# Optimization experiments

Measured on AMD Instinct MI355X. Metric: run time of the kernel, lower is better.

## Reference

```python
import jax, jax.numpy as jnp
import numpy as np

TQ, TK, B, QD, KD, VD = 1024, 1024, 16, 1024, 1024, 1024

def setup_inputs() -> dict:
    key = jax.random.key(0)
    k1, k2, k3, k4, k5 = jax.random.split(key, 5)
    queries = jax.random.normal(k1, (TQ, B, QD), dtype=jnp.float32)
    keys = jax.random.normal(k2, (TK, B, KD), dtype=jnp.float32)
    values = jax.random.normal(k3, (TK, B, VD), dtype=jnp.float32)
    # torch Linear weight [out=key_dim, in=query_dim], uniform(-0.1, 0.1)
    W = jax.random.uniform(k4, (KD, QD), dtype=jnp.float32, minval=-0.1, maxval=0.1)
    # mask: True means position is masked out (filled with -inf)
    mask = jax.random.bernoulli(k5, 0.5, (TK, B))
    return {"queries": queries, "keys": keys, "values": values, "W": W, "mask": mask}

def reference(queries, keys, values, W, mask):
    # project queries: [Tq,B,QD] @ W.T -> [Tq,B,KD]
    q = jnp.einsum('tbq,kq->tbk', queries, W)
    # scores: [B,Tq,Tk]
    scores = jnp.einsum('tbk,sbk->bts', q, keys)
    # mask [Tk,B] -> [B,1,Tk]; True positions get -inf
    scores = jnp.where(mask.T[:, None, :], -jnp.inf, scores)
    attn = jax.nn.softmax(scores, axis=-1)  # [B,Tq,Tk]
    # output: [B,Tq,Vd] -> [Tq,B,Vd]
    x = jnp.einsum('bts,sbv->tbv', attn, values)
    # attn returned as [Tq,B,Tk] (matches torch .transpose(0,1))
    return x, jnp.transpose(attn, (1, 0, 2))
```

## Files before the change

kernel.cpp:

```cpp
#include <hip/hip_runtime.h>
#include <stdint.h>

#define TQd 1024
#define TKd 1024
#define Bd  16
#define QDd 1024
#define KDd 1024
#define VDd 1024
#define MROWS (TQd * Bd)

#define S_W   326390.0f
#define S_QIN 5021.4f
#define S_KIN 5021.4f
#define S_QP  2719.9f

typedef float f32x4 __attribute__((ext_vector_type(4)));
typedef short short8 __attribute__((ext_vector_type(8)));
typedef unsigned short u16x4 __attribute__((ext_vector_type(4)));
typedef int i32x4 __attribute__((ext_vector_type(4)));
typedef signed char i8x4 __attribute__((ext_vector_type(4)));

__device__ __forceinline__ unsigned short f2bf(float x) {
  unsigned u = __float_as_uint(x);
  u += 0x7FFFu + ((u >> 16) & 1u);
  return (unsigned short)(u >> 16);
}
__device__ __forceinline__ float bf2f(unsigned short h) {
  return __uint_as_float(((unsigned)h) << 16);
}

__device__ __forceinline__ char* lds_ptr(unsigned short* base, int r, int kcol) {
  int byte = (r << 7) + (kcol << 1);
  byte ^= (r & 7) << 4;
  return (char*)base + byte;
}
__device__ __forceinline__ i32x4 lds_fragi(const char* plane, int row, int chunk) {
  return *(const i32x4*)(plane + row * 128 + (((chunk) ^ (row & 7)) << 4));
}
__device__ __forceinline__ short8 lds_fragh(const char* plane, int row, int chunk) {
  return *(const short8*)(plane + row * 128 + (((chunk) ^ (row & 7)) << 4));
}

__device__ __forceinline__ void gload16(const void* g, void* l) {
  __builtin_amdgcn_global_load_lds(
      (const __attribute__((address_space(1))) void*)(uintptr_t)g,
      (__attribute__((address_space(3))) void*)(uintptr_t)l,
      16, 0, 0);
}

#define MFMA_BF16 __builtin_amdgcn_mfma_f32_16x16x32_bf16
#define MFMA_I8   __builtin_amdgcn_mfma_i32_16x16x64_i8
#define SBAR() __builtin_amdgcn_s_barrier()

__device__ __forceinline__ void q16split(float x, float scale, int& hi, int& lo) {
  float r = rintf(x * scale);
  r = fminf(fmaxf(r, -32639.f), 32639.f);
  int ri = (int)r;
  lo = (int)(signed char)(ri & 255);
  hi = (ri - lo) >> 8;
}

__global__ __launch_bounds__(256) void k_quant8(const float* __restrict__ src,
                                                signed char* __restrict__ hi,
                                                signed char* __restrict__ lo,
                                                int n4, float scale) {
  int i = blockIdx.x * 256 + threadIdx.x;
  int stride = gridDim.x * 256;
  for (; i < n4; i += stride) {
    f32x4 v = ((const f32x4*)src)[i];
    i8x4 h, l;
#pragma unroll
    for (int j = 0; j < 4; ++j) {
      int hj, lj;
      q16split(v[j], scale, hj, lj);
      h[j] = (signed char)hj;
      l[j] = (signed char)lj;
    }
    ((i8x4*)hi)[i] = h;
    ((i8x4*)lo)[i] = l;
  }
}

__global__ __launch_bounds__(256) void k_vt(const float* __restrict__ values,
                                            unsigned short* __restrict__ vt) {
  __shared__ unsigned short T[64 * 64];
  const int tid = threadIdx.x;
  const int b = blockIdx.z;
  const int s0 = blockIdx.y * 64, v0 = blockIdx.x * 64;
  const int sIdx = tid >> 4, vIdx = tid & 15;
  f32x4 rv[4];
#pragma unroll
  for (int j = 0; j < 4; ++j)
    rv[j] = *(const f32x4*)(values + (size_t)(s0 + sIdx * 4 + j) * (Bd * VDd) +
                            (size_t)b * VDd + v0 + vIdx * 4);
#pragma unroll
  for (int j2 = 0; j2 < 4; ++j2) {
    u16x4 w;
    w[0] = f2bf(rv[0][j2]); w[1] = f2bf(rv[1][j2]);
    w[2] = f2bf(rv[2][j2]); w[3] = f2bf(rv[3][j2]);
    int v = vIdx * 4 + j2;
    int byte = (v << 7) + (sIdx << 3);
    byte ^= (v & 7) << 4;
    *(u16x4*)((char*)T + byte) = w;
  }
  __syncthreads();
  const int l15 = tid & 15, lk = (tid >> 4) & 3, wv = tid >> 6;
  int row = wv * 16 + l15;
#pragma unroll
  for (int c = 0; c < 2; ++c) {
    int lc = lk + c * 4;
    int byte = (row << 7) + (((lc) ^ (row & 7)) << 4);
    short8 d = *(const short8*)((char*)T + byte);
    *(short8*)(vt + ((size_t)(b * 1024 + v0 + row)) * 1024 + s0 + lc * 8) = d;
  }
}

__device__ __forceinline__ void stage2_i8c(char* p, int kt,
    const signed char* ah, const signed char* al,
    const signed char* bh, const signed char* bl,
    int m0, int n0, int wv, int lane) {
  int rsub = lane >> 3;
  int lc = (lane & 7) ^ rsub;
  const signed char* A = (lc < 4) ? ah : al;
  const signed char* B = (lc < 4) ? bh : bl;
  int ke = kt + (lc & 3) * 16;
#pragma unroll
  for (int i = 0; i < 4; ++i) {
    int issue = wv * 4 + i;
    int row = issue * 8 + rsub;
    gload16(A + (size_t)(m0 + row) * 1024 + ke, p + issue * 1024);
    gload16(B + (size_t)(n0 + row) * 1024 + ke, p + 16384 + issue * 1024);
  }
}

__device__ __forceinline__ void stage2_i8s(char* p, int kt,
    const signed char* ah, const signed char* al,
    const signed char* bh, const signed char* bl,
    int t0, int s0, int b, int wv, int lane) {
  int rsub = lane >> 3;
  int lc = (lane & 7) ^ rsub;
  const signed char* A = (lc < 4) ? ah : al;
  const signed char* B = (lc < 4) ? bh : bl;
  int ke = kt + (lc & 3) * 16;
#pragma unroll
  for (int i = 0; i < 4; ++i) {
    int issue = wv * 4 + i;
    int row = issue * 8 + rsub;
    gload16(A + ((size_t)(t0 + row) * Bd + b) * 1024 + ke, p + issue * 1024);
    gload16(B + ((size_t)(s0 + row) * Bd + b) * 1024 + ke, p + 16384 + issue * 1024);
  }
}

#define GEMMI8_LOOP2(STAGEM)                                                  \
  const int tid = threadIdx.x;                                                \
  const int lane = tid & 63, wv = tid >> 6;                                   \
  const int wm = wv >> 1, wn = wv & 1;                                        \
  const int l15 = lane & 15, lk = lane >> 4;                                  \
  const i32x4 izero = {0, 0, 0, 0};                                           \
  i32x4 acc1[4][4], acc2[4][4];                                               \
  _Pragma("unroll") for (int m = 0; m < 4; ++m)                               \
  _Pragma("unroll") for (int n = 0; n < 4; ++n) {                             \
    acc1[m][n] = izero; acc2[m][n] = izero;                                   \
  }                                                                           \
  char* p0 = ldsbuf;                                                          \
  char* p1 = ldsbuf + 32768;                                                  \
  STAGEM(p0, 0);                                                              \
  asm volatile("s_waitcnt vmcnt(0)" ::: "memory");                            \
  SBAR();                                                                     \
  _Pragma("unroll 1") for (int h = 0; h < 16; ++h) {                          \
    if (h < 15) STAGEM(p1, (h + 1) * 64);                                     \
    i32x4 bh_[4], bl_[4], ah_[4], al_[4];                                     \
    _Pragma("unroll") for (int n = 0; n < 4; ++n) {                           \
      bh_[n] = lds_fragi(p0 + 16384, wn * 64 + n * 16 + l15, lk);             \
      bl_[n] = lds_fragi(p0 + 16384, wn * 64 + n * 16 + l15, 4 + lk);         \
    }                                                                         \
    _Pragma("unroll") for (int m = 0; m < 4; ++m) {                           \
      ah_[m] = lds_fragi(p0, wm * 64 + m * 16 + l15, lk);                     \
      al_[m] = lds_fragi(p0, wm * 64 + m * 16 + l15, 4 + lk);                 \
    }                                                                         \
    __builtin_amdgcn_s_setprio(1);                                            \
    _Pragma("unroll") for (int m = 0; m < 4; ++m)                             \
    _Pragma("unroll") for (int n = 0; n < 4; ++n) {                           \
      acc1[m][n] = MFMA_I8(ah_[m], bh_[n], acc1[m][n], 0, 0, 0);              \
      acc2[m][n] = MFMA_I8(ah_[m], bl_[n], acc2[m][n], 0, 0, 0);              \
      acc2[m][n] = MFMA_I8(al_[m], bh_[n], acc2[m][n], 0, 0, 0);              \
    }                                                                         \
    __builtin_amdgcn_s_setprio(0);                                            \
    if (h < 15) {                                                             \
      asm volatile("s_waitcnt vmcnt(0)" ::: "memory");                        \
      SBAR();                                                                 \
      char* pt = p0; p0 = p1; p1 = pt;                                        \
    }                                                                         \
  }

__global__ __launch_bounds__(256, 2) void k_qproj_i8(
    const signed char* __restrict__ Qh, const signed char* __restrict__ Ql,
    const signed char* __restrict__ Wh, const signed char* __restrict__ Wl,
    signed char* __restrict__ qh, signed char* __restrict__ ql) {
  __shared__ char ldsbuf[2 * 32768];
  int lin = blockIdx.x;
  int x = lin & 7, c = lin >> 3;
  const int m0 = (x * 16 + (c >> 3)) * 128, n0 = (c & 7) * 128;
#define STG_Q(P, KT) stage2_i8c(P, KT, Qh, Ql, Wh, Wl, m0, n0, wv, lane)
  GEMMI8_LOOP2(STG_Q)
#undef STG_Q
  const float inv = 1.0f / (S_QIN * S_W);
#pragma unroll
  for (int m = 0; m < 4; ++m)
#pragma unroll
    for (int n = 0; n < 4; ++n)
#pragma unroll
      for (int r = 0; r < 4; ++r) {
        int row = m0 + wm * 64 + m * 16 + lk * 4 + r;
        int col = n0 + wn * 64 + n * 16 + l15;
        float q = ((float)acc1[m][n][r] * 65536.f + (float)acc2[m][n][r] * 256.f) * inv;
        int hj, lj;
        q16split(q, S_QP, hj, lj);
        qh[(size_t)row * KDd + col] = (signed char)hj;
        ql[(size_t)row * KDd + col] = (signed char)lj;
      }
}

__global__ __launch_bounds__(256, 2) void k_scores_i8(
    const signed char* __restrict__ qh, const signed char* __restrict__ ql,
    const signed char* __restrict__ kh, const signed char* __restrict__ kl,
    float* __restrict__ sc) {
  __shared__ char ldsbuf[2 * 32768];
  int lin = blockIdx.x;
  int x = lin & 7, c = lin >> 3;
  const int b = x * 2 + (c >> 6);
  const int t0 = ((c >> 3) & 7) * 128, s0 = (c & 7) * 128;
#define STG_S(P, KT) stage2_i8s(P, KT, qh, ql, kh, kl, t0, s0, b, wv, lane)
  GEMMI8_LOOP2(STG_S)
#undef STG_S
  const float inv = 1.0f / (S_QP * S_KIN);
#pragma unroll
  for (int m = 0; m < 4; ++m)
#pragma unroll
    for (int n = 0; n < 4; ++n)
#pragma unroll
      for (int r = 0; r < 4; ++r) {
        int t = t0 + wm * 64 + m * 16 + lk * 4 + r;
        int s = s0 + wn * 64 + n * 16 + l15;
        float v = ((float)acc1[m][n][r] * 65536.f + (float)acc2[m][n][r] * 256.f) * inv;
        sc[((size_t)t * Bd + b) * TKd + s] = v;
      }
}

__global__ __launch_bounds__(256) void k_softmax2(float* __restrict__ attn,
                                                  const int* __restrict__ mask,
                                                  unsigned short* __restrict__ pb) {
  const int wv = threadIdx.x >> 6, lane = threadIdx.x & 63;
  const size_t r = (size_t)blockIdx.x * 4 + wv;
  const int b = (int)(r & 15);
  float* row = attn + r * TKd;
  unsigned short* prow = pb + r * TKd;

  f32x4 v[4];
  float m = -INFINITY;
#pragma unroll
  for (int c = 0; c < 4; ++c) {
    int s0 = (c * 64 + lane) * 4;
    v[c] = *(const f32x4*)(row + s0);
#pragma unroll
    for (int j = 0; j < 4; ++j) {
      if (mask[(size_t)(s0 + j) * Bd + b] != 0) v[c][j] = -INFINITY;
      m = fmaxf(m, v[c][j]);
    }
  }
#pragma unroll
  for (int off = 32; off > 0; off >>= 1) m = fmaxf(m, __shfl_xor(m, off));
  float sum = 0.f;
#pragma unroll
  for (int c = 0; c < 4; ++c)
#pragma unroll
    for (int j = 0; j < 4; ++j) {
      float e = expf(v[c][j] - m);
      v[c][j] = e;
      sum += e;
    }
#pragma unroll
  for (int off = 32; off > 0; off >>= 1) sum += __shfl_xor(sum, off);
  float inv = 1.f / sum;
#pragma unroll
  for (int c = 0; c < 4; ++c) {
    int s0 = (c * 64 + lane) * 4;
    u16x4 hb;
#pragma unroll
    for (int j = 0; j < 4; ++j) {
      v[c][j] *= inv;
      hb[j] = f2bf(v[c][j]);
    }
    *(f32x4*)(row + s0) = v[c];
    *(u16x4*)(prow + s0) = hb;
  }
}

__device__ __forceinline__ void stage2_pv(char* p, int st,
    const unsigned short* pb, const unsigned short* vtb,
    int t0, int v0, int b, int wv, int lane) {
  int rsub = lane >> 3;
  int lc = (lane & 7) ^ rsub;
  int ke = st + lc * 8;
#pragma unroll
  for (int i = 0; i < 4; ++i) {
    int issue = wv * 4 + i;
    int row = issue * 8 + rsub;
    gload16(pb + ((size_t)(t0 + row) * Bd + b) * 1024 + ke, p + issue * 1024);
    gload16(vtb + (size_t)(v0 + row) * 1024 + ke, p + 16384 + issue * 1024);
  }
}

__global__ __launch_bounds__(256, 2) void k_out3(const unsigned short* __restrict__ pb,
                                                 const unsigned short* __restrict__ vt,
                                                 float* __restrict__ xo) {
  __shared__ char ldsbuf[2 * 32768];
  int lin = blockIdx.x;
  int x = lin & 7, c = lin >> 3;
  const int b = x * 2 + (c >> 6);
  const int t0 = ((c >> 3) & 7) * 128, v0 = (c & 7) * 128;
  const unsigned short* vtb = vt + (size_t)b * VDd * TKd;

  const int tid = threadIdx.x;
  const int lane = tid & 63, wv = tid >> 6;
  const int wm = wv >> 1, wn = wv & 1;
  const int l15 = lane & 15, lk = lane >> 4;
  const f32x4 vzero = {0.f, 0.f, 0.f, 0.f};
  f32x4 acc[4][4];
#pragma unroll
  for (int m = 0; m < 4; ++m)
#pragma unroll
    for (int n = 0; n < 4; ++n) acc[m][n] = vzero;

  char* p0 = ldsbuf;
  char* p1 = ldsbuf + 32768;
#define STG_PV(P, ST) stage2_pv(P, ST, pb, vtb, t0, v0, b, wv, lane)
  STG_PV(p0, 0);
  asm volatile("s_waitcnt vmcnt(0)" ::: "memory");
  SBAR();
#pragma unroll 1
  for (int h = 0; h < 16; ++h) {
    if (h < 15) STG_PV(p1, (h + 1) * 64);
    short8 bf[4][2], af[4][2];
#pragma unroll
    for (int n = 0; n < 4; ++n)
#pragma unroll
      for (int kk = 0; kk < 2; ++kk)
        bf[n][kk] = lds_fragh(p0 + 16384, wn * 64 + n * 16 + l15, kk * 4 + lk);
#pragma unroll
    for (int m = 0; m < 4; ++m)
#pragma unroll
      for (int kk = 0; kk < 2; ++kk)
        af[m][kk] = lds_fragh(p0, wm * 64 + m * 16 + l15, kk * 4 + lk);
    __builtin_amdgcn_s_setprio(1);
#pragma unroll
    for (int m = 0; m < 4; ++m)
#pragma unroll
      for (int n = 0; n < 4; ++n)
#pragma unroll
        for (int kk = 0; kk < 2; ++kk)
          acc[m][n] = MFMA_BF16(af[m][kk], bf[n][kk], acc[m][n], 0, 0, 0);
    __builtin_amdgcn_s_setprio(0);
    if (h < 15) {
      asm volatile("s_waitcnt vmcnt(0)" ::: "memory");
      SBAR();
      char* pt = p0; p0 = p1; p1 = pt;
    }
  }
#undef STG_PV
#pragma unroll
  for (int m = 0; m < 4; ++m)
#pragma unroll
    for (int n = 0; n < 4; ++n)
#pragma unroll
      for (int r = 0; r < 4; ++r) {
        int t = t0 + wm * 64 + m * 16 + lk * 4 + r;
        int vcol = v0 + wn * 64 + n * 16 + l15;
        xo[((size_t)t * Bd + b) * VDd + vcol] = acc[m][n][r];
      }
}

__global__ __launch_bounds__(256) void k_qproj(const float* __restrict__ A,
                                               const float* __restrict__ Wm,
                                               unsigned short* __restrict__ qh,
                                               unsigned short* __restrict__ ql) {
  __shared__ unsigned short Ah[128 * 64], Al[128 * 64], Bh[128 * 64], Bl[128 * 64];
  const int tid = threadIdx.x;
  const int m0 = blockIdx.y * 128, n0 = blockIdx.x * 128;
  const int lane = tid & 63, wv = tid >> 6;
  const int wr = (wv >> 1) * 64, wc = (wv & 1) * 64;
  const int l15 = lane & 15, lk = lane >> 4;
  const f32x4 vzero = {0.f, 0.f, 0.f, 0.f};
  f32x4 acc[4][4];
#pragma unroll
  for (int m = 0; m < 4; ++m)
#pragma unroll
    for (int n = 0; n < 4; ++n) acc[m][n] = vzero;
  for (int kt = 0; kt < QDd; kt += 64) {
    __syncthreads();
#pragma unroll
    for (int i = 0; i < 8; ++i) {
      int slot = i * 256 + tid;
      int r = slot >> 4, c = (slot & 15) * 4;
      f32x4 va = *(const f32x4*)(A + (size_t)(m0 + r) * QDd + kt + c);
      f32x4 vb = *(const f32x4*)(Wm + (size_t)(n0 + r) * QDd + kt + c);
      u16x4 ha, la, hb, lb;
#pragma unroll
      for (int j = 0; j < 4; ++j) {
        ha[j] = f2bf(va[j]); la[j] = f2bf(va[j] - bf2f(ha[j]));
        hb[j] = f2bf(vb[j]); lb[j] = f2bf(vb[j] - bf2f(hb[j]));
      }
      *(u16x4*)lds_ptr(Ah, r, c) = ha;
      *(u16x4*)lds_ptr(Al, r, c) = la;
      *(u16x4*)lds_ptr(Bh, r, c) = hb;
      *(u16x4*)lds_ptr(Bl, r, c) = lb;
    }
    __syncthreads();
#pragma unroll
    for (int kk = 0; kk < 2; ++kk) {
      short8 ah[4], al[4], bh[4], bl[4];
#pragma unroll
      for (int m = 0; m < 4; ++m) {
        ah[m] = *(const short8*)lds_ptr(Ah, wr + m * 16 + l15, kk * 32 + lk * 8);
        al[m] = *(const short8*)lds_ptr(Al, wr + m * 16 + l15, kk * 32 + lk * 8);
      }
#pragma unroll
      for (int n = 0; n < 4; ++n) {
        bh[n] = *(const short8*)lds_ptr(Bh, wc + n * 16 + l15, kk * 32 + lk * 8);
        bl[n] = *(const short8*)lds_ptr(Bl, wc + n * 16 + l15, kk * 32 + lk * 8);
      }
#pragma unroll
      for (int m = 0; m < 4; ++m)
#pragma unroll
        for (int n = 0; n < 4; ++n) {
          acc[m][n] = MFMA_BF16(ah[m], bh[n], acc[m][n], 0, 0, 0);
          acc[m][n] = MFMA_BF16(ah[m], bl[n], acc[m][n], 0, 0, 0);
          acc[m][n] = MFMA_BF16(al[m], bh[n], acc[m][n], 0, 0, 0);
        }
    }
  }
#pragma unroll
  for (int m = 0; m < 4; ++m)
#pragma unroll
    for (int n = 0; n < 4; ++n)
#pragma unroll
      for (int r = 0; r < 4; ++r) {
        int row = m0 + wr + m * 16 + lk * 4 + r;
        int col = n0 + wc + n * 16 + l15;
        float v = acc[m][n][r];
        unsigned short h = f2bf(v);
        qh[(size_t)row * KDd + col] = h;
        ql[(size_t)row * KDd + col] = f2bf(v - bf2f(h));
      }
}

__global__ __launch_bounds__(256) void k_scores(const unsigned short* __restrict__ qh,
                                                const unsigned short* __restrict__ ql,
                                                const float* __restrict__ keys,
                                                float* __restrict__ sc) {
  __shared__ unsigned short Ah[128 * 64], Al[128 * 64], Bh[128 * 64], Bl[128 * 64];
  const int tid = threadIdx.x;
  const int b = blockIdx.z;
  const int t0 = blockIdx.y * 128, s0 = blockIdx.x * 128;
  const int lane = tid & 63, wv = tid >> 6;
  const int wr = (wv >> 1) * 64, wc = (wv & 1) * 64;
  const int l15 = lane & 15, lk = lane >> 4;
  const f32x4 vzero = {0.f, 0.f, 0.f, 0.f};
  f32x4 acc[4][4];
#pragma unroll
  for (int m = 0; m < 4; ++m)
#pragma unroll
    for (int n = 0; n < 4; ++n) acc[m][n] = vzero;
  for (int kt = 0; kt < KDd; kt += 64) {
    __syncthreads();
#pragma unroll
    for (int i = 0; i < 4; ++i) {
      int slot = i * 256 + tid;
      int r = slot >> 3, c = (slot & 7) * 8;
      size_t off = (size_t)(t0 + r) * (Bd * KDd) + (size_t)b * KDd + kt + c;
      *(short8*)lds_ptr(Ah, r, c) = *(const short8*)(qh + off);
      *(short8*)lds_ptr(Al, r, c) = *(const short8*)(ql + off);
    }
#pragma unroll
    for (int i = 0; i < 8; ++i) {
      int slot = i * 256 + tid;
      int r = slot >> 4, c = (slot & 15) * 4;
      f32x4 v = *(const f32x4*)(keys + (size_t)(s0 + r) * (Bd * KDd) + (size_t)b * KDd + kt + c);
      u16x4 h, l;
#pragma unroll
      for (int j = 0; j < 4; ++j) {
        h[j] = f2bf(v[j]); l[j] = f2bf(v[j] - bf2f(h[j]));
      }
      *(u16x4*)lds_ptr(Bh, r, c) = h;
      *(u16x4*)lds_ptr(Bl, r, c) = l;
    }
    __syncthreads();
#pragma unroll
    for (int kk = 0; kk < 2; ++kk) {
      short8 ah[4], al[4], bh[4], bl[4];
#pragma unroll
      for (int m = 0; m < 4; ++m) {
        ah[m] = *(const short8*)lds_ptr(Ah, wr + m * 16 + l15, kk * 32 + lk * 8);
        al[m] = *(const short8*)lds_ptr(Al, wr + m * 16 + l15, kk * 32 + lk * 8);
      }
#pragma unroll
      for (int n = 0; n < 4; ++n) {
        bh[n] = *(const short8*)lds_ptr(Bh, wc + n * 16 + l15, kk * 32 + lk * 8);
        bl[n] = *(const short8*)lds_ptr(Bl, wc + n * 16 + l15, kk * 32 + lk * 8);
      }
#pragma unroll
      for (int m = 0; m < 4; ++m)
#pragma unroll
        for (int n = 0; n < 4; ++n) {
          acc[m][n] = MFMA_BF16(ah[m], bh[n], acc[m][n], 0, 0, 0);
          acc[m][n] = MFMA_BF16(ah[m], bl[n], acc[m][n], 0, 0, 0);
          acc[m][n] = MFMA_BF16(al[m], bh[n], acc[m][n], 0, 0, 0);
        }
    }
  }
#pragma unroll
  for (int m = 0; m < 4; ++m)
#pragma unroll
    for (int n = 0; n < 4; ++n)
#pragma unroll
      for (int r = 0; r < 4; ++r) {
        int t = t0 + wr + m * 16 + lk * 4 + r;
        int s = s0 + wc + n * 16 + l15;
        sc[(size_t)t * (Bd * TKd) + (size_t)b * TKd + s] = acc[m][n][r];
      }
}

__global__ __launch_bounds__(256) void k_softmax(float* __restrict__ attn,
                                                 const int* __restrict__ mask) {
  const int wv = threadIdx.x >> 6, lane = threadIdx.x & 63;
  const size_t r = (size_t)blockIdx.x * 4 + wv;
  const int b = (int)(r & 15);
  float* row = attn + r * TKd;
  f32x4 v[4];
  float m = -INFINITY;
#pragma unroll
  for (int c = 0; c < 4; ++c) {
    int s0 = (c * 64 + lane) * 4;
    v[c] = *(const f32x4*)(row + s0);
#pragma unroll
    for (int j = 0; j < 4; ++j) {
      if (mask[(size_t)(s0 + j) * Bd + b] != 0) v[c][j] = -INFINITY;
      m = fmaxf(m, v[c][j]);
    }
  }
#pragma unroll
  for (int off = 32; off > 0; off >>= 1) m = fmaxf(m, __shfl_xor(m, off));
  float sum = 0.f;
#pragma unroll
  for (int c = 0; c < 4; ++c)
#pragma unroll
    for (int j = 0; j < 4; ++j) {
      float e = expf(v[c][j] - m);
      v[c][j] = e;
      sum += e;
    }
#pragma unroll
  for (int off = 32; off > 0; off >>= 1) sum += __shfl_xor(sum, off);
  float inv = 1.f / sum;
#pragma unroll
  for (int c = 0; c < 4; ++c) {
    int s0 = (c * 64 + lane) * 4;
#pragma unroll
    for (int j = 0; j < 4; ++j) v[c][j] *= inv;
    *(f32x4*)(row + s0) = v[c];
  }
}

__global__ __launch_bounds__(256) void k_out(const float* __restrict__ attn,
                                             const float* __restrict__ values,
                                             float* __restrict__ xo) {
  __shared__ unsigned short Ph[128 * 64], Vt[128 * 64];
  const int tid = threadIdx.x;
  const int b = blockIdx.z;
  const int t0 = blockIdx.y * 128, v0 = blockIdx.x * 128;
  const int lane = tid & 63, wv = tid >> 6;
  const int wr = (wv >> 1) * 64, wc = (wv & 1) * 64;
  const int l15 = lane & 15, lk = lane >> 4;
  const f32x4 vzero = {0.f, 0.f, 0.f, 0.f};
  f32x4 acc[4][4];
#pragma unroll
  for (int m = 0; m < 4; ++m)
#pragma unroll
    for (int n = 0; n < 4; ++n) acc[m][n] = vzero;
  for (int st = 0; st < TKd; st += 64) {
    __syncthreads();
#pragma unroll
    for (int i = 0; i < 8; ++i) {
      int slot = i * 256 + tid;
      int r = slot >> 4, c = (slot & 15) * 4;
      f32x4 p = *(const f32x4*)(attn + (size_t)(t0 + r) * (Bd * TKd) + (size_t)b * TKd + st + c);
      u16x4 h;
#pragma unroll
      for (int j = 0; j < 4; ++j) h[j] = f2bf(p[j]);
      *(u16x4*)lds_ptr(Ph, r, c) = h;
    }
#pragma unroll
    for (int i = 0; i < 2; ++i) {
      int blk = i * 256 + tid;
      int vb = blk & 31, sb = blk >> 5;
      int v4 = vb * 4, s4 = sb * 4;
      f32x4 rv[4];
#pragma unroll
      for (int j = 0; j < 4; ++j)
        rv[j] = *(const f32x4*)(values + (size_t)(st + s4 + j) * (Bd * VDd) + (size_t)b * VDd + v0 + v4);
#pragma unroll
      for (int j = 0; j < 4; ++j) {
        u16x4 w;
        w[0] = f2bf(rv[0][j]); w[1] = f2bf(rv[1][j]);
        w[2] = f2bf(rv[2][j]); w[3] = f2bf(rv[3][j]);
        *(u16x4*)lds_ptr(Vt, v4 + j, s4) = w;
      }
    }
    __syncthreads();
#pragma unroll
    for (int kk = 0; kk < 2; ++kk) {
      short8 a[4], bv[4];
#pragma unroll
      for (int m = 0; m < 4; ++m)
        a[m] = *(const short8*)lds_ptr(Ph, wr + m * 16 + l15, kk * 32 + lk * 8);
#pragma unroll
      for (int n = 0; n < 4; ++n)
        bv[n] = *(const short8*)lds_ptr(Vt, wc + n * 16 + l15, kk * 32 + lk * 8);
#pragma unroll
      for (int m = 0; m < 4; ++m)
#pragma unroll
        for (int n = 0; n < 4; ++n)
          acc[m][n] = MFMA_BF16(a[m], bv[n], acc[m][n], 0, 0, 0);
    }
  }
#pragma unroll
  for (int m = 0; m < 4; ++m)
#pragma unroll
    for (int n = 0; n < 4; ++n)
#pragma unroll
      for (int r = 0; r < 4; ++r) {
        int t = t0 + wr + m * 16 + lk * 4 + r;
        int vcol = v0 + wc + n * 16 + l15;
        xo[(size_t)t * (Bd * VDd) + (size_t)b * VDd + vcol] = acc[m][n][r];
      }
}

extern "C" void kernel_launch(void* const* d_in, const int* in_sizes, int n_in,
                              void* d_out, int out_size, void* d_ws, size_t ws_size,
                              hipStream_t stream) {
  const float* queries = (const float*)d_in[0];
  const float* keys    = (const float*)d_in[1];
  const float* values  = (const float*)d_in[2];
  const float* W       = (const float*)d_in[3];
  const int*   mask    = (const int*)d_in[4];

  float* x_out    = (float*)d_out;
  float* attn_out = x_out + (size_t)MROWS * TKd;

  const size_t need = 130ull << 20;
  if (ws_size >= need) {
    signed char* wh8 = (signed char*)d_ws;
    signed char* wl8 = wh8 + (size_t)KDd * QDd;
    signed char* kh8 = wl8 + (size_t)KDd * QDd;
    signed char* kl8 = kh8 + (size_t)MROWS * KDd;
    signed char* Qh8 = kl8 + (size_t)MROWS * KDd;
    signed char* Ql8 = Qh8 + (size_t)MROWS * QDd;
    signed char* qh8 = Ql8 + (size_t)MROWS * QDd;
    signed char* ql8 = qh8 + (size_t)MROWS * KDd;
    unsigned short* vt16 = (unsigned short*)(ql8 + (size_t)MROWS * KDd);
    unsigned short* pb = (unsigned short*)Qh8;

    k_quant8<<<1024, 256, 0, stream>>>(W, wh8, wl8, (KDd * QDd) / 4, S_W);
    k_quant8<<<2048, 256, 0, stream>>>(keys, kh8, kl8, (MROWS * KDd) / 4, S_KIN);
    k_quant8<<<2048, 256, 0, stream>>>(queries, Qh8, Ql8, (MROWS * QDd) / 4, S_QIN);
    k_vt<<<dim3(VDd / 64, TKd / 64, Bd), 256, 0, stream>>>(values, vt16);
    k_qproj_i8<<<1024, 256, 0, stream>>>(Qh8, Ql8, wh8, wl8, qh8, ql8);
    k_scores_i8<<<1024, 256, 0, stream>>>(qh8, ql8, kh8, kl8, attn_out);
    k_softmax2<<<MROWS / 4, 256, 0, stream>>>(attn_out, mask, pb);
    k_out3<<<1024, 256, 0, stream>>>(pb, vt16, x_out);
  } else {
    unsigned short* qh = (unsigned short*)d_ws;
    unsigned short* ql = qh + (size_t)MROWS * KDd;
    k_qproj<<<dim3(KDd / 128, MROWS / 128), 256, 0, stream>>>(queries, W, qh, ql);
    k_scores<<<dim3(TKd / 128, TQd / 128, Bd), 256, 0, stream>>>(qh, ql, keys, attn_out);
    k_softmax<<<MROWS / 4, 256, 0, stream>>>(attn_out, mask);
    k_out<<<dim3(VDd / 128, TQd / 128, Bd), 256, 0, stream>>>(attn_out, values, x_out);
  }
}
```

Baseline: 269.4 us.

## Fuse prep kernels into one launch and switch int8 GEMMs to 32x32x32 MFMA

Merges the three quantization launches and the values transpose into a single k_prep kernel, using block-index ranges to pick the region each block handles. This removes launch gaps and tail idle time between the small prep kernels. The two int8 GEMM kernels (query projection and scores) move from 16x16x64 MFMA tiles to 32x32x32 MFMA tiles with 16-wide accumulators, which reduces LDS fragment reads per MFMA. The epilogue row and column mapping is rewritten to match the 32x32 output layout. The larger accumulators may raise register pressure and change the global store pattern.

New measurement: 273.5 us. About the same (+1.5%).

```diff
diff --git a/kernel.cpp b/kernel.cpp
--- a/kernel.cpp
+++ b/kernel.cpp
@@ -18,6 +18,7 @@
 typedef short short8 __attribute__((ext_vector_type(8)));
 typedef unsigned short u16x4 __attribute__((ext_vector_type(4)));
 typedef int i32x4 __attribute__((ext_vector_type(4)));
+typedef int i32x16 __attribute__((ext_vector_type(16)));
 typedef signed char i8x4 __attribute__((ext_vector_type(4)));
 
 __device__ __forceinline__ unsigned short f2bf(float x) {
@@ -49,7 +50,7 @@
 }
 
 #define MFMA_BF16 __builtin_amdgcn_mfma_f32_16x16x32_bf16
-#define MFMA_I8   __builtin_amdgcn_mfma_i32_16x16x64_i8
+#define MFMA_I8_32 __builtin_amdgcn_mfma_i32_32x32x32_i8
 #define SBAR() __builtin_amdgcn_s_barrier()
 
 __device__ __forceinline__ void q16split(float x, float scale, int& hi, int& lo) {
@@ -60,12 +61,13 @@
   hi = (ri - lo) >> 8;
 }
 
-__global__ __launch_bounds__(256) void k_quant8(const float* __restrict__ src,
-                                                signed char* __restrict__ hi,
-                                                signed char* __restrict__ lo,
-                                                int n4, float scale) {
-  int i = blockIdx.x * 256 + threadIdx.x;
-  int stride = gridDim.x * 256;
+__device__ __forceinline__ void quant_region(const float* __restrict__ src,
+                                             signed char* __restrict__ hi,
+                                             signed char* __restrict__ lo,
+                                             int n4, float scale,
+                                             int relblk, int nblk, int tid) {
+  int i = relblk * 256 + tid;
+  int stride = nblk * 256;
   for (; i < n4; i += stride) {
     f32x4 v = ((const f32x4*)src)[i];
     i8x4 h, l;
@@ -81,37 +83,51 @@
   }
 }
 
-__global__ __launch_bounds__(256) void k_vt(const float* __restrict__ values,
-                                            unsigned short* __restrict__ vt) {
+__global__ __launch_bounds__(256) void k_prep(
+    const float* __restrict__ W, const float* __restrict__ keys,
+    const float* __restrict__ queries, const float* __restrict__ values,
+    signed char* __restrict__ wh, signed char* __restrict__ wl,
+    signed char* __restrict__ kh, signed char* __restrict__ kl,
+    signed char* __restrict__ Qh, signed char* __restrict__ Ql,
+    unsigned short* __restrict__ vt) {
   __shared__ unsigned short T[64 * 64];
+  const int bid = blockIdx.x;
   const int tid = threadIdx.x;
-  const int b = blockIdx.z;
-  const int s0 = blockIdx.y * 64, v0 = blockIdx.x * 64;
-  const int sIdx = tid >> 4, vIdx = tid & 15;
-  f32x4 rv[4];
-#pragma unroll
-  for (int j = 0; j < 4; ++j)
-    rv[j] = *(const f32x4*)(values + (size_t)(s0 + sIdx * 4 + j) * (Bd * VDd) +
-                            (size_t)b * VDd + v0 + vIdx * 4);
-#pragma unroll
-  for (int j2 = 0; j2 < 4; ++j2) {
-    u16x4 w;
-    w[0] = f2bf(rv[0][j2]); w[1] = f2bf(rv[1][j2]);
-    w[2] = f2bf(rv[2][j2]); w[3] = f2bf(rv[3][j2]);
-    int v = vIdx * 4 + j2;
-    int byte = (v << 7) + (sIdx << 3);
-    byte ^= (v & 7) << 4;
-    *(u16x4*)((char*)T + byte) = w;
-  }
-  __syncthreads();
-  const int l15 = tid & 15, lk = (tid >> 4) & 3, wv = tid >> 6;
-  int row = wv * 16 + l15;
-#pragma unroll
-  for (int c = 0; c < 2; ++c) {
-    int lc = lk + c * 4;
-    int byte = (row << 7) + (((lc) ^ (row & 7)) << 4);
-    short8 d = *(const short8*)((char*)T + byte);
-    *(short8*)(vt + ((size_t)(b * 1024 + v0 + row)) * 1024 + s0 + lc * 8) = d;
+  if (bid < 256) {
+    quant_region(W, wh, wl, (KDd * QDd) / 4, S_W, bid, 256, tid);
+  } else if (bid < 2048) {
+    quant_region(keys, kh, kl, (MROWS * KDd) / 4, S_KIN, bid - 256, 1792, tid);
+  } else if (bid < 3840) {
+    quant_region(queries, Qh, Ql, (MROWS * QDd) / 4, S_QIN, bid - 2048, 1792, tid);
+  } else {
+    int rel = bid - 3840;
+    const int v0 = (rel & 15) * 64, s0 = ((rel >> 4) & 15) * 64, b = rel >> 8;
+    const int sIdx = tid >> 4, vIdx = tid & 15;
+    f32x4 rv[4];
+#pragma unroll
+    for (int j = 0; j < 4; ++j)
+      rv[j] = *(const f32x4*)(values + (size_t)(s0 + sIdx * 4 + j) * (Bd * VDd) +
+                              (size_t)b * VDd + v0 + vIdx * 4);
+#pragma unroll
+    for (int j2 = 0; j2 < 4; ++j2) {
+      u16x4 w;
+      w[0] = f2bf(rv[0][j2]); w[1] = f2bf(rv[1][j2]);
+      w[2] = f2bf(rv[2][j2]); w[3] = f2bf(rv[3][j2]);
+      int v = vIdx * 4 + j2;
+      int byte = (v << 7) + (sIdx << 3);
+      byte ^= (v & 7) << 4;
+      *(u16x4*)((char*)T + byte) = w;
+    }
+    __syncthreads();
+    const int l15 = tid & 15, lk = (tid >> 4) & 3, wv = tid >> 6;
+    int row = wv * 16 + l15;
+#pragma unroll
+    for (int c = 0; c < 2; ++c) {
+      int lc = lk + c * 4;
+      int byte = (row << 7) + (((lc) ^ (row & 7)) << 4);
+      short8 d = *(const short8*)((char*)T + byte);
+      *(short8*)(vt + ((size_t)(b * 1024 + v0 + row)) * 1024 + s0 + lc * 8) = d;
+    }
   }
 }
 
@@ -151,16 +167,15 @@
   }
 }
 
-#define GEMMI8_LOOP2(STAGEM)                                                  \
+#define GEMMI8_LOOP3(STAGEM)                                                  \
   const int tid = threadIdx.x;                                                \
   const int lane = tid & 63, wv = tid >> 6;                                   \
   const int wm = wv >> 1, wn = wv & 1;                                        \
-  const int l15 = lane & 15, lk = lane >> 4;                                  \
-  const i32x4 izero = {0, 0, 0, 0};                                           \
-  i32x4 acc1[4][4], acc2[4][4];                                               \
-  _Pragma("unroll") for (int m = 0; m < 4; ++m)                               \
-  _Pragma("unroll") for (int n = 0; n < 4; ++n) {                             \
-    acc1[m][n] = izero; acc2[m][n] = izero;                                   \
+  const int l31 = lane & 31, lg = lane >> 5;                                  \
+  i32x16 acc1[2][2], acc2[2][2];                                              \
+  _Pragma("unroll") for (int m = 0; m < 2; ++m)                               \
+  _Pragma("unroll") for (int n = 0; n < 2; ++n) {                             \
+    acc1[m][n] = (i32x16)(0); acc2[m][n] = (i32x16)(0);                       \
   }                                                                           \
   char* p0 = ldsbuf;                                                          \
   char* p1 = ldsbuf + 32768;                                                  \
@@ -169,21 +184,21 @@
   SBAR();                                                                     \
   _Pragma("unroll 1") for (int h = 0; h < 16; ++h) {                          \
     if (h < 15) STAGEM(p1, (h + 1) * 64);                                     \
-    i32x4 bh_[4], bl_[4], ah_[4], al_[4];                                     \
-    _Pragma("unroll") for (int n = 0; n < 4; ++n) {                           \
-      bh_[n] = lds_fragi(p0 + 16384, wn * 64 + n * 16 + l15, lk);             \
-      bl_[n] = lds_fragi(p0 + 16384, wn * 64 + n * 16 + l15, 4 + lk);         \
-    }                                                                         \
-    _Pragma("unroll") for (int m = 0; m < 4; ++m) {                           \
-      ah_[m] = lds_fragi(p0, wm * 64 + m * 16 + l15, lk);                     \
-      al_[m] = lds_fragi(p0, wm * 64 + m * 16 + l15, 4 + lk);                 \
+    i32x4 a_h[2][2], a_l[2][2], b_h[2][2], b_l[2][2];                         \
+    _Pragma("unroll") for (int ks = 0; ks < 2; ++ks)                          \
+    _Pragma("unroll") for (int t = 0; t < 2; ++t) {                           \
+      a_h[t][ks] = lds_fragi(p0, wm * 64 + t * 32 + l31, 2 * ks + lg);        \
+      a_l[t][ks] = lds_fragi(p0, wm * 64 + t * 32 + l31, 4 + 2 * ks + lg);    \
+      b_h[t][ks] = lds_fragi(p0 + 16384, wn * 64 + t * 32 + l31, 2 * ks + lg);\
+      b_l[t][ks] = lds_fragi(p0 + 16384, wn * 64 + t * 32 + l31, 4 + 2 * ks + lg);\
     }                                                                         \
     __builtin_amdgcn_s_setprio(1);                                            \
-    _Pragma("unroll") for (int m = 0; m < 4; ++m)                             \
-    _Pragma("unroll") for (int n = 0; n < 4; ++n) {                           \
-      acc1[m][n] = MFMA_I8(ah_[m], bh_[n], acc1[m][n], 0, 0, 0);              \
-      acc2[m][n] = MFMA_I8(ah_[m], bl_[n], acc2[m][n], 0, 0, 0);              \
-      acc2[m][n] = MFMA_I8(al_[m], bh_[n], acc2[m][n], 0, 0, 0);              \
+    _Pragma("unroll") for (int mt = 0; mt < 2; ++mt)                          \
+    _Pragma("unroll") for (int nt = 0; nt < 2; ++nt)                          \
+    _Pragma("unroll") for (int ks = 0; ks < 2; ++ks) {                        \
+      acc1[mt][nt] = MFMA_I8_32(a_h[mt][ks], b_h[nt][ks], acc1[mt][nt], 0, 0, 0);\
+      acc2[mt][nt] = MFMA_I8_32(a_h[mt][ks], b_l[nt][ks], acc2[mt][nt], 0, 0, 0);\
+      acc2[mt][nt] = MFMA_I8_32(a_l[mt][ks], b_h[nt][ks], acc2[mt][nt], 0, 0, 0);\
     }                                                                         \
     __builtin_amdgcn_s_setprio(0);                                            \
     if (h < 15) {                                                             \
@@ -202,18 +217,19 @@
   int x = lin & 7, c = lin >> 3;
   const int m0 = (x * 16 + (c >> 3)) * 128, n0 = (c & 7) * 128;
 #define STG_Q(P, KT) stage2_i8c(P, KT, Qh, Ql, Wh, Wl, m0, n0, wv, lane)
-  GEMMI8_LOOP2(STG_Q)
+  GEMMI8_LOOP3(STG_Q)
 #undef STG_Q
   const float inv = 1.0f / (S_QIN * S_W);
 #pragma unroll
-  for (int m = 0; m < 4; ++m)
-#pragma unroll
-    for (int n = 0; n < 4; ++n)
-#pragma unroll
-      for (int r = 0; r < 4; ++r) {
-        int row = m0 + wm * 64 + m * 16 + lk * 4 + r;
-        int col = n0 + wn * 64 + n * 16 + l15;
-        float q = ((float)acc1[m][n][r] * 65536.f + (float)acc2[m][n][r] * 256.f) * inv;
+  for (int mt = 0; mt < 2; ++mt)
+#pragma unroll
+    for (int nt = 0; nt < 2; ++nt)
+#pragma unroll
+      for (int r = 0; r < 16; ++r) {
+        int row = m0 + wm * 64 + mt * 32 + (r & 3) + 8 * (r >> 2) + 4 * lg;
+        int col = n0 + wn * 64 + nt * 32 + l31;
+        float q = ((float)acc1[mt][nt][r] * 65536.f +
+                   (float)acc2[mt][nt][r] * 256.f) * inv;
         int hj, lj;
         q16split(q, S_QP, hj, lj);
         qh[(size_t)row * KDd + col] = (signed char)hj;
@@ -231,18 +247,19 @@
   const int b = x * 2 + (c >> 6);
   const int t0 = ((c >> 3) & 7) * 128, s0 = (c & 7) * 128;
 #define STG_S(P, KT) stage2_i8s(P, KT, qh, ql, kh, kl, t0, s0, b, wv, lane)
-  GEMMI8_LOOP2(STG_S)
+  GEMMI8_LOOP3(STG_S)
 #undef STG_S
   const float inv = 1.0f / (S_QP * S_KIN);
 #pragma unroll
-  for (int m = 0; m < 4; ++m)
-#pragma unroll
-    for (int n = 0; n < 4; ++n)
-#pragma unroll
-      for (int r = 0; r < 4; ++r) {
-        int t = t0 + wm * 64 + m * 16 + lk * 4 + r;
-        int s = s0 + wn * 64 + n * 16 + l15;
-        float v = ((float)acc1[m][n][r] * 65536.f + (float)acc2[m][n][r] * 256.f) * inv;
+  for (int mt = 0; mt < 2; ++mt)
+#pragma unroll
+    for (int nt = 0; nt < 2; ++nt)
+#pragma unroll
+      for (int r = 0; r < 16; ++r) {
+        int t = t0 + wm * 64 + mt * 32 + (r & 3) + 8 * (r >> 2) + 4 * lg;
+        int s = s0 + wn * 64 + nt * 32 + l31;
+        float v = ((float)acc1[mt][nt][r] * 65536.f +
+                   (float)acc2[mt][nt][r] * 256.f) * inv;
         sc[((size_t)t * Bd + b) * TKd + s] = v;
       }
 }
@@ -670,10 +687,8 @@
     unsigned short* vt16 = (unsigned short*)(ql8 + (size_t)MROWS * KDd);
     unsigned short* pb = (unsigned short*)Qh8;
 
-    k_quant8<<<1024, 256, 0, stream>>>(W, wh8, wl8, (KDd * QDd) / 4, S_W);
-    k_quant8<<<2048, 256, 0, stream>>>(keys, kh8, kl8, (MROWS * KDd) / 4, S_KIN);
-    k_quant8<<<2048, 256, 0, stream>>>(queries, Qh8, Ql8, (MROWS * QDd) / 4, S_QIN);
-    k_vt<<<dim3(VDd / 64, TKd / 64, Bd), 256, 0, stream>>>(values, vt16);
+    k_prep<<<7936, 256, 0, stream>>>(W, keys, queries, values,
+                                     wh8, wl8, kh8, kl8, Qh8, Ql8, vt16);
     k_qproj_i8<<<1024, 256, 0, stream>>>(Qh8, Ql8, wh8, wl8, qh8, ql8);
     k_scores_i8<<<1024, 256, 0, stream>>>(qh8, ql8, kh8, kl8, attn_out);
     k_softmax2<<<MROWS / 4, 256, 0, stream>>>(attn_out, mask, pb);
```
